# Performance work log

Measured on AMD Instinct MI355X. Metric: run time of the kernel, lower is better.

## Reference

```python
import jax, jax.numpy as jnp
import numpy as np

MARGIN = 0.8  # TripletMarginMiner(margin=0.8, type_of_triplets='semihard')
Z_DIM = 512
N_CONCEPT = 64
NUM_TASK, NUM_SHOT, NUM_WAY = 16, 5, 5


def _triplet_indices(num_shot, num_way):
    # labels = torch.arange(num_way).repeat(num_shot) -> tile pattern
    labels = np.tile(np.arange(num_way), num_shot)
    N = labels.shape[0]
    same = labels[:, None] == labels[None, :]
    pos = same & ~np.eye(N, dtype=bool)          # a != p, same label
    neg = ~same                                  # different label
    a, p, n = np.nonzero(pos[:, :, None] & neg[:, None, :])  # all candidate triplets
    return jnp.asarray(a), jnp.asarray(p), jnp.asarray(n)


def setup_inputs() -> dict:
    key = jax.random.key(0)
    ks = jax.random.split(key, 12)
    d = Z_DIM
    s = lambda fan: 1.0 / np.sqrt(fan)
    inp = {
        'input_data': jax.random.normal(ks[0], (NUM_TASK, NUM_SHOT, NUM_WAY, d), jnp.float32),
        # proj_inner: Linear(3d -> 2d), ReLU, Linear(2d -> d)
        'W1': jax.random.normal(ks[1], (3 * d, 2 * d), jnp.float32) * s(3 * d),
        'b1': jnp.zeros((2 * d,), jnp.float32),
        'W2': jax.random.normal(ks[2], (2 * d, d), jnp.float32) * s(2 * d),
        'b2': jnp.zeros((d,), jnp.float32),
        # proj_outer: Linear(d -> 2d), ReLU, Linear(2d -> d)
        'W3': jax.random.normal(ks[3], (d, 2 * d), jnp.float32) * s(d),
        'b3': jnp.zeros((2 * d,), jnp.float32),
        'W4': jax.random.normal(ks[4], (2 * d, d), jnp.float32) * s(2 * d),
        'b4': jnp.zeros((d,), jnp.float32),
        # cls: Linear(d -> n_concept)
        'Wc': jax.random.normal(ks[5], (d, N_CONCEPT), jnp.float32) * s(d),
        'bc': jnp.zeros((N_CONCEPT,), jnp.float32),
    }
    return inp


def reference(input_data, W1, b1, W2, b2, W3, b3, W4, b4, Wc, bc):
    num_task, num_shot, num_way, d = input_data.shape
    x = input_data.reshape(num_task, num_shot * num_way, d)  # [K, N, d]
    a, p, n = _triplet_indices(num_shot, num_way)            # fixed triplet set [T]

    # --- semihard mining (no grad; binary mask so no grad path anyway) ---
    # LpDistance default: normalize embeddings, then L2 distance
    xn = x / jnp.linalg.norm(x, axis=-1, keepdims=True)
    sq = jnp.sum(xn * xn, axis=-1)                           # [K, N]
    D2 = sq[:, :, None] + sq[:, None, :] - 2.0 * jnp.einsum('kid,kjd->kij', xn, xn)
    D = jnp.sqrt(jnp.clip(D2, 0.0))                          # [K, N, N]
    tm = D[:, a, n] - D[:, a, p]                             # an_dist - ap_dist, [K, T]
    mask = ((tm > 0.0) & (tm <= MARGIN)).astype(x.dtype)     # semihard: 0 < margin <= 0.8

    # --- gather triplet embeddings (unnormalized), concat [x_a, x_p, x_n] ---
    feat = jnp.concatenate([x[:, a], x[:, p], x[:, n]], axis=-1)  # [K, T, 3d]

    # proj_inner then masked sum over mined triplets per task
    h = jax.nn.relu(feat @ W1 + b1) @ W2 + b2                # [K, T, d]
    pooled = jnp.einsum('ktd,kt->kd', h, mask)               # [K, d]

    o = jax.nn.relu(pooled @ W3 + b3) @ W4 + b4              # [K, d]
    score = o @ Wc + bc                                      # [K, n_concept]
    return jax.nn.softmax(score, axis=-1)
```

## Files before the change

### kernel.cpp

```cpp
#include <hip/hip_runtime.h>
#include <math.h>

#define NT 16
#define NR 25
#define DZ 512
#define D2Z 1024
#define NC 64

typedef short bf16x8 __attribute__((ext_vector_type(8)));
typedef float f32x4  __attribute__((ext_vector_type(4)));

#define TP  76
#define XSP 520
#define CP  68

static __device__ inline unsigned short f2bf(float v) {
    union { float f; unsigned u; } x; x.f = v;
    unsigned r = x.u + 0x7fffu + ((x.u >> 16) & 1u);
    return (unsigned short)(r >> 16);
}
static __device__ inline float bf2f(unsigned short h) {
    union { float f; unsigned u; } x; x.u = ((unsigned)h) << 16; return x.f;
}

__global__ __launch_bounds__(256) void k_prep(
    const float* __restrict__ x, const float* __restrict__ W1,
    unsigned short* __restrict__ W1h, unsigned short* __restrict__ W1l,
    float* __restrict__ Dm)
{
    __shared__ unsigned short th[64 * TP], tl[64 * TP];
    int vb = blockIdx.x;
    int tid = threadIdx.x;

    if (vb < 384) {
        int jt = vb & 15;
        int rs = vb >> 4;
        int r0 = rs * 64;
        int j0 = jt * 64;
        int c  = r0 >> 9;
        int rb = r0 & 511;

        #pragma unroll
        for (int it = 0; it < 4; it++) {
            int rl = (tid >> 4) + it * 16;
            int jj = (tid & 15) * 4;
            float4 v = *(const float4*)(W1 + (size_t)(r0 + rl) * D2Z + j0 + jj);
            unsigned short h0 = f2bf(v.x), h1 = f2bf(v.y), h2 = f2bf(v.z), h3 = f2bf(v.w);
            th[rl * TP + jj + 0] = h0; tl[rl * TP + jj + 0] = f2bf(v.x - bf2f(h0));
            th[rl * TP + jj + 1] = h1; tl[rl * TP + jj + 1] = f2bf(v.y - bf2f(h1));
            th[rl * TP + jj + 2] = h2; tl[rl * TP + jj + 2] = f2bf(v.z - bf2f(h2));
            th[rl * TP + jj + 3] = h3; tl[rl * TP + jj + 3] = f2bf(v.w - bf2f(h3));
        }
        __syncthreads();

        #pragma unroll
        for (int it = 0; it < 4; it++) {
            int jl = (tid >> 4) + it * 16;
            int r4 = (tid & 15) * 4;
            ushort4 hv = make_ushort4(th[(r4+0)*TP + jl], th[(r4+1)*TP + jl],
                                      th[(r4+2)*TP + jl], th[(r4+3)*TP + jl]);
            ushort4 lv = make_ushort4(tl[(r4+0)*TP + jl], tl[(r4+1)*TP + jl],
                                      tl[(r4+2)*TP + jl], tl[(r4+3)*TP + jl]);
            size_t dst = ((size_t)c * D2Z + j0 + jl) * DZ + rb + r4;
            *(ushort4*)(W1h + dst) = hv;
            *(ushort4*)(W1l + dst) = lv;
        }
    } else {
        int i = vb - 384;
        int k = i & 15, a = i >> 4;
        int lane = tid & 63;
        int w    = tid >> 6;
        const float* xk = x + (size_t)k * NR * DZ;

        const float4* xap = (const float4*)(xk + a * DZ);
        float4 a0 = xap[lane];
        float4 a1 = xap[lane + 64];

        float sa = a0.x*a0.x + a0.y*a0.y + a0.z*a0.z + a0.w*a0.w
                 + a1.x*a1.x + a1.y*a1.y + a1.z*a1.z + a1.w*a1.w;
        #pragma unroll
        for (int off = 32; off; off >>= 1) sa += __shfl_xor(sa, off);
        float inva = 1.0f / sqrtf(sa);
        a0.x *= inva; a0.y *= inva; a0.z *= inva; a0.w *= inva;
        a1.x *= inva; a1.y *= inva; a1.z *= inva; a1.w *= inva;
        float sqa = a0.x*a0.x + a0.y*a0.y + a0.z*a0.z + a0.w*a0.w
                  + a1.x*a1.x + a1.y*a1.y + a1.z*a1.z + a1.w*a1.w;
        #pragma unroll
        for (int off = 32; off; off >>= 1) sqa += __shfl_xor(sqa, off);

        for (int j = w; j < NR; j += 4) {
            const float4* xjp = (const float4*)(xk + j * DZ);
            float4 j0 = xjp[lane];
            float4 j1 = xjp[lane + 64];
            float sj = j0.x*j0.x + j0.y*j0.y + j0.z*j0.z + j0.w*j0.w
                     + j1.x*j1.x + j1.y*j1.y + j1.z*j1.z + j1.w*j1.w;
            #pragma unroll
            for (int off = 32; off; off >>= 1) sj += __shfl_xor(sj, off);
            float invj = 1.0f / sqrtf(sj);
            j0.x *= invj; j0.y *= invj; j0.z *= invj; j0.w *= invj;
            j1.x *= invj; j1.y *= invj; j1.z *= invj; j1.w *= invj;

            float sqj = j0.x*j0.x + j0.y*j0.y + j0.z*j0.z + j0.w*j0.w
                      + j1.x*j1.x + j1.y*j1.y + j1.z*j1.z + j1.w*j1.w;
            float dij = a0.x*j0.x + a0.y*j0.y + a0.z*j0.z + a0.w*j0.w
                      + a1.x*j1.x + a1.y*j1.y + a1.z*j1.z + a1.w*j1.w;
            #pragma unroll
            for (int off = 32; off; off >>= 1) {
                sqj += __shfl_xor(sqj, off);
                dij += __shfl_xor(dij, off);
            }
            float d2 = sqa + sqj - 2.0f * dij;
            float d  = sqrtf(fmaxf(d2, 0.0f));
            if (lane == 0) Dm[((size_t)k * NR + a) * NR + j] = d;
        }
    }
}

__global__ __launch_bounds__(1024) void k_fused(
    const float* __restrict__ x,
    const unsigned short* __restrict__ W1h, const unsigned short* __restrict__ W1l,
    const float* __restrict__ b1, const float* __restrict__ Dm,
    float* __restrict__ G, float* __restrict__ cnt)
{
    __shared__ unsigned short xs_h[25 * XSP], xs_l[25 * XSP];
    __shared__ float Ct[4][75 * CP];
    __shared__ float Dm_s[NR * NR];
    __shared__ float red[16][64];
    __shared__ float cred[4];

    int bid = blockIdx.x;
    int k  = bid >> 4;
    int jt = bid & 15;
    int j0 = jt * 64;

    int tid  = threadIdx.x;
    int lane = tid & 63;
    int w    = tid >> 6;
    int g    = w & 3;
    int kh   = w >> 2;
    int q    = lane >> 4;
    int ln16 = lane & 15;

    for (int idx = tid; idx < NR * NR; idx += 1024)
        Dm_s[idx] = Dm[(size_t)k * NR * NR + idx];

    for (int gi = tid; gi < NR * 64; gi += 1024) {
        int row = gi >> 6;
        int c8  = (gi & 63) * 8;
        const float* xp = x + ((size_t)k * NR + row) * DZ + c8;
        float4 v0 = *(const float4*)(xp);
        float4 v1 = *(const float4*)(xp + 4);
        unsigned short h;
        ushort4 ha, hb, la, lb;
        h = f2bf(v0.x); ha.x = h; la.x = f2bf(v0.x - bf2f(h));
        h = f2bf(v0.y); ha.y = h; la.y = f2bf(v0.y - bf2f(h));
        h = f2bf(v0.z); ha.z = h; la.z = f2bf(v0.z - bf2f(h));
        h = f2bf(v0.w); ha.w = h; la.w = f2bf(v0.w - bf2f(h));
        h = f2bf(v1.x); hb.x = h; lb.x = f2bf(v1.x - bf2f(h));
        h = f2bf(v1.y); hb.y = h; lb.y = f2bf(v1.y - bf2f(h));
        h = f2bf(v1.z); hb.z = h; lb.z = f2bf(v1.z - bf2f(h));
        h = f2bf(v1.w); hb.w = h; lb.w = f2bf(v1.w - bf2f(h));
        *(ushort4*)&xs_h[row * XSP + c8]     = ha;
        *(ushort4*)&xs_h[row * XSP + c8 + 4] = hb;
        *(ushort4*)&xs_l[row * XSP + c8]     = la;
        *(ushort4*)&xs_l[row * XSP + c8 + 4] = lb;
    }
    __syncthreads();

    if (jt == 0 && tid < 256) {
        float cntv = 0.0f;
        for (int idx = tid; idx < 2000; idx += 256) {
            int a   = idx / 80;
            int rem = idx - a * 80;
            int mi  = rem / 20;
            int nn  = rem - mi * 20;
            int qa = a % 5, mdiv = a / 5;
            int m = mi + (mi >= mdiv);
            int p = qa + 5 * m;
            int ng = nn >> 2, o = nn & 3;
            int n = ng * 5 + o + (o >= qa);
            float tm = Dm_s[a * NR + n] - Dm_s[a * NR + p];
            cntv += ((tm > 0.0f) && (tm <= 0.8f)) ? 1.0f : 0.0f;
        }
        #pragma unroll
        for (int off = 32; off; off >>= 1) cntv += __shfl_xor(cntv, off);
        if (lane == 0) cred[w] = cntv;
    }

    int rowA1 = 16 + ln16;
    if (rowA1 > 24) rowA1 = 24;

    const unsigned short* wb_h = W1h + ((size_t)j0 + g * 16 + ln16) * DZ + q * 8;
    const unsigned short* wb_l = W1l + ((size_t)j0 + g * 16 + ln16) * DZ + q * 8;

    for (int c = 0; c < 3; c++) {
        f32x4 acc0 = (f32x4){0.f,0.f,0.f,0.f};
        f32x4 acc1 = (f32x4){0.f,0.f,0.f,0.f};
        const unsigned short* wch = wb_h + (size_t)c * D2Z * DZ;
        const unsigned short* wcl = wb_l + (size_t)c * D2Z * DZ;

        #pragma unroll
        for (int kc2 = 0; kc2 < 4; kc2++) {
            int kc  = kh * 4 + kc2;
            int kog = kc * 32 + q * 8;
            bf16x8 b_h = *(const bf16x8*)(wch + kc * 32);
            bf16x8 b_l = *(const bf16x8*)(wcl + kc * 32);
            bf16x8 a0h = *(const bf16x8*)&xs_h[ln16 * XSP + kog];
            bf16x8 a0l = *(const bf16x8*)&xs_l[ln16 * XSP + kog];
            bf16x8 a1h = *(const bf16x8*)&xs_h[rowA1 * XSP + kog];
            bf16x8 a1l = *(const bf16x8*)&xs_l[rowA1 * XSP + kog];
            acc0 = __builtin_amdgcn_mfma_f32_16x16x32_bf16(a0h, b_h, acc0, 0, 0, 0);
            acc0 = __builtin_amdgcn_mfma_f32_16x16x32_bf16(a0h, b_l, acc0, 0, 0, 0);
            acc0 = __builtin_amdgcn_mfma_f32_16x16x32_bf16(a0l, b_h, acc0, 0, 0, 0);
            acc1 = __builtin_amdgcn_mfma_f32_16x16x32_bf16(a1h, b_h, acc1, 0, 0, 0);
            acc1 = __builtin_amdgcn_mfma_f32_16x16x32_bf16(a1h, b_l, acc1, 0, 0, 0);
            acc1 = __builtin_amdgcn_mfma_f32_16x16x32_bf16(a1l, b_h, acc1, 0, 0, 0);
        }

        int col = g * 16 + ln16;
        #pragma unroll
        for (int r = 0; r < 4; r++) {
            int r0 = q * 4 + r;
            Ct[kh][(c * 25 + r0) * CP + col] = acc0[r];
            int r1 = 16 + q * 4 + r;
            if (r1 < 25) Ct[kh][(c * 25 + r1) * CP + col] = acc1[r];
        }
    }
    __syncthreads();

    if (jt == 0 && tid == 0)
        cnt[k] = cred[0] + cred[1] + cred[2] + cred[3];

    int j  = tid & 63;
    int h  = (tid >> 6) & 3;
    int ag = tid >> 8;
    float b1v = b1[j0 + j];

    float a3v[NR];
    #pragma unroll
    for (int i = 0; i < NR; i++)
        a3v[i] = Ct[0][(50 + i) * CP + j] + Ct[1][(50 + i) * CP + j]
               + Ct[2][(50 + i) * CP + j] + Ct[3][(50 + i) * CP + j];

    float acc = 0.0f;
    #define ACC_BODY(a) { \
        const int qa = (a) % 5, mdiv = (a) / 5; \
        int m = h + (h >= mdiv); \
        int p = qa + 5 * m; \
        float a1v = Ct[0][(a) * CP + j] + Ct[1][(a) * CP + j] \
                  + Ct[2][(a) * CP + j] + Ct[3][(a) * CP + j]; \
        float a2v = Ct[0][(25 + p) * CP + j] + Ct[1][(25 + p) * CP + j] \
                  + Ct[2][(25 + p) * CP + j] + Ct[3][(25 + p) * CP + j]; \
        float dap = Dm_s[(a) * NR + p]; \
        float s = a1v + a2v + b1v; \
        _Pragma("unroll") \
        for (int ng = 0; ng < 5; ng++) { \
            _Pragma("unroll") \
            for (int o = 0; o < 4; o++) { \
                int n = ng * 5 + o + (o >= qa); \
                float tm = Dm_s[(a) * NR + n] - dap; \
                bool sel = (tm > 0.0f) && (tm <= 0.8f); \
                float pre = fmaxf(s + a3v[n], 0.0f); \
                acc = fmaf(sel ? 1.0f : 0.0f, pre, acc); \
            } \
        } }
    if (ag == 0) {
        #pragma unroll
        for (int a = 0; a < 7; a++) ACC_BODY(a)
    } else if (ag == 1) {
        #pragma unroll
        for (int a = 7; a < 13; a++) ACC_BODY(a)
    } else if (ag == 2) {
        #pragma unroll
        for (int a = 13; a < 19; a++) ACC_BODY(a)
    } else {
        #pragma unroll
        for (int a = 19; a < 25; a++) ACC_BODY(a)
    }
    #undef ACC_BODY

    red[tid >> 6][j] = acc;
    __syncthreads();
    if (tid < 64) {
        float s = 0.0f;
        #pragma unroll
        for (int r = 0; r < 16; r++) s += red[r][tid];
        G[(size_t)k * D2Z + j0 + tid] = s;
    }
}


__global__ __launch_bounds__(256) void kA(const float* __restrict__ G,
                                          const float* __restrict__ W2,
                                          float* __restrict__ pp)
{
    __shared__ float GsT[64 * 16];
    __shared__ float red2[4][16][64];
    int jq = blockIdx.x & 15, ct = blockIdx.x >> 4;
    int tid = threadIdx.x;

    for (int idx = tid; idx < 1024; idx += 256) {
        int t = idx & 15, jj = idx >> 4;
        GsT[jj * 16 + t] = G[(size_t)t * D2Z + jq * 64 + jj];
    }
    __syncthreads();

    int cg = tid & 63, sub = tid >> 6;
    int col = ct * 64 + cg;
    float acc[16];
    #pragma unroll
    for (int t = 0; t < 16; t++) acc[t] = 0.0f;

    for (int jj = 0; jj < 16; jj++) {
        int jr = sub * 16 + jj;
        float wv = W2[(size_t)(jq * 64 + jr) * DZ + col];
        const float4* gp = (const float4*)&GsT[jr * 16];
        float4 g0 = gp[0], g1 = gp[1], g2 = gp[2], g3 = gp[3];
        acc[0]  = fmaf(g0.x, wv, acc[0]);  acc[1]  = fmaf(g0.y, wv, acc[1]);
        acc[2]  = fmaf(g0.z, wv, acc[2]);  acc[3]  = fmaf(g0.w, wv, acc[3]);
        acc[4]  = fmaf(g1.x, wv, acc[4]);  acc[5]  = fmaf(g1.y, wv, acc[5]);
        acc[6]  = fmaf(g1.z, wv, acc[6]);  acc[7]  = fmaf(g1.w, wv, acc[7]);
        acc[8]  = fmaf(g2.x, wv, acc[8]);  acc[9]  = fmaf(g2.y, wv, acc[9]);
        acc[10] = fmaf(g2.z, wv, acc[10]); acc[11] = fmaf(g2.w, wv, acc[11]);
        acc[12] = fmaf(g3.x, wv, acc[12]); acc[13] = fmaf(g3.y, wv, acc[13]);
        acc[14] = fmaf(g3.z, wv, acc[14]); acc[15] = fmaf(g3.w, wv, acc[15]);
    }
    #pragma unroll
    for (int t = 0; t < 16; t++) red2[sub][t][cg] = acc[t];
    __syncthreads();
    for (int r = 0; r < 4; r++) {
        int oi = tid + r * 256;
        int t = oi >> 6, c2 = oi & 63;
        float s = red2[0][t][c2] + red2[1][t][c2] + red2[2][t][c2] + red2[3][t][c2];
        pp[(size_t)jq * 8192 + t * DZ + ct * 64 + c2] = s;
    }
}

__global__ __launch_bounds__(256) void kB(const float* __restrict__ pp,
                                          const float* __restrict__ cnt,
                                          const float* __restrict__ b2,
                                          const float* __restrict__ W3,
                                          float* __restrict__ up)
{
    __shared__ float PsT[64 * 16];
    __shared__ float red2[4][16][64];
    int ct = blockIdx.x & 15, cq = blockIdx.x >> 4;
    int tid = threadIdx.x;

    for (int idx = tid; idx < 1024; idx += 256) {
        int t = idx & 15, cl = idx >> 4;
        int c = cq * 64 + cl;
        float v = cnt[t] * b2[c];
        #pragma unroll
        for (int sl = 0; sl < 16; sl++)
            v += pp[(size_t)sl * 8192 + t * DZ + c];
        PsT[cl * 16 + t] = v;
    }
    __syncthreads();

    int cg = tid & 63, sub = tid >> 6;
    int col = ct * 64 + cg;
    float acc[16];
    #pragma unroll
    for (int t = 0; t < 16; t++) acc[t] = 0.0f;

    for (int cl = 0; cl < 16; cl++) {
        int cr = sub * 16 + cl;
        float wv = W3[(size_t)(cq * 64 + cr) * D2Z + col];
        const float4* gp = (const float4*)&PsT[cr * 16];
        float4 g0 = gp[0], g1 = gp[1], g2 = gp[2], g3 = gp[3];
        acc[0]  = fmaf(g0.x, wv, acc[0]);  acc[1]  = fmaf(g0.y, wv, acc[1]);
        acc[2]  = fmaf(g0.z, wv, acc[2]);  acc[3]  = fmaf(g0.w, wv, acc[3]);
        acc[4]  = fmaf(g1.x, wv, acc[4]);  acc[5]  = fmaf(g1.y, wv, acc[5]);
        acc[6]  = fmaf(g1.z, wv, acc[6]);  acc[7]  = fmaf(g1.w, wv, acc[7]);
        acc[8]  = fmaf(g2.x, wv, acc[8]);  acc[9]  = fmaf(g2.y, wv, acc[9]);
        acc[10] = fmaf(g2.z, wv, acc[10]); acc[11] = fmaf(g2.w, wv, acc[11]);
        acc[12] = fmaf(g3.x, wv, acc[12]); acc[13] = fmaf(g3.y, wv, acc[13]);
        acc[14] = fmaf(g3.z, wv, acc[14]); acc[15] = fmaf(g3.w, wv, acc[15]);
    }
    #pragma unroll
    for (int t = 0; t < 16; t++) red2[sub][t][cg] = acc[t];
    __syncthreads();
    for (int r = 0; r < 4; r++) {
        int oi = tid + r * 256;
        int t = oi >> 6, c2 = oi & 63;
        float s = red2[0][t][c2] + red2[1][t][c2] + red2[2][t][c2] + red2[3][t][c2];
        up[(size_t)cq * 16384 + t * D2Z + ct * 64 + c2] = s;
    }
}

__global__ __launch_bounds__(256) void kC(const float* __restrict__ up,
                                          const float* __restrict__ b3,
                                          const float* __restrict__ W4,
                                          float* __restrict__ op)
{
    __shared__ float UsT[64 * 16];
    __shared__ float red2[4][16][64];
    int ct = blockIdx.x & 7, sq = blockIdx.x >> 3;
    int tid = threadIdx.x;

    for (int idx = tid; idx < 1024; idx += 256) {
        int t = idx & 15, sl = idx >> 4;
        int s = sq * 64 + sl;
        float v = b3[s];
        #pragma unroll
        for (int c8 = 0; c8 < 8; c8++)
            v += up[(size_t)c8 * 16384 + t * D2Z + s];
        UsT[sl * 16 + t] = fmaxf(v, 0.0f);
    }
    __syncthreads();

    int cg = tid & 63, sub = tid >> 6;
    int col = ct * 64 + cg;
    float acc[16];
    #pragma unroll
    for (int t = 0; t < 16; t++) acc[t] = 0.0f;

    for (int sl = 0; sl < 16; sl++) {
        int sr = sub * 16 + sl;
        float wv = W4[(size_t)(sq * 64 + sr) * DZ + col];
        const float4* gp = (const float4*)&UsT[sr * 16];
        float4 g0 = gp[0], g1 = gp[1], g2 = gp[2], g3 = gp[3];
        acc[0]  = fmaf(g0.x, wv, acc[0]);  acc[1]  = fmaf(g0.y, wv, acc[1]);
        acc[2]  = fmaf(g0.z, wv, acc[2]);  acc[3]  = fmaf(g0.w, wv, acc[3]);
        acc[4]  = fmaf(g1.x, wv, acc[4]);  acc[5]  = fmaf(g1.y, wv, acc[5]);
        acc[6]  = fmaf(g1.z, wv, acc[6]);  acc[7]  = fmaf(g1.w, wv, acc[7]);
        acc[8]  = fmaf(g2.x, wv, acc[8]);  acc[9]  = fmaf(g2.y, wv, acc[9]);
        acc[10] = fmaf(g2.z, wv, acc[10]); acc[11] = fmaf(g2.w, wv, acc[11]);
        acc[12] = fmaf(g3.x, wv, acc[12]); acc[13] = fmaf(g3.y, wv, acc[13]);
        acc[14] = fmaf(g3.z, wv, acc[14]); acc[15] = fmaf(g3.w, wv, acc[15]);
    }
    #pragma unroll
    for (int t = 0; t < 16; t++) red2[sub][t][cg] = acc[t];
    __syncthreads();
    for (int r = 0; r < 4; r++) {
        int oi = tid + r * 256;
        int t = oi >> 6, c2 = oi & 63;
        float s = red2[0][t][c2] + red2[1][t][c2] + red2[2][t][c2] + red2[3][t][c2];
        op[(size_t)sq * 8192 + t * DZ + ct * 64 + c2] = s;
    }
}

__global__ __launch_bounds__(256) void kD(const float* __restrict__ op,
                                          const float* __restrict__ b4,
                                          const float* __restrict__ Wc,
                                          const float* __restrict__ bc,
                                          float* __restrict__ out)
{
    __shared__ float Os[DZ];
    __shared__ float tmp[4][64];
    int k = blockIdx.x;
    int tid = threadIdx.x;

    for (int c = tid; c < DZ; c += 256) {
        float v = b4[c];
        #pragma unroll
        for (int sl = 0; sl < 16; sl++)
            v += op[(size_t)sl * 8192 + k * DZ + c];
        Os[c] = v;
    }
    __syncthreads();

    int oc = tid & 63, seg = tid >> 6;
    float a0 = 0.f, a1 = 0.f, a2 = 0.f, a3 = 0.f;
    int r0 = seg * 128;
    #pragma unroll 4
    for (int rr = r0; rr < r0 + 128; rr += 4) {
        a0 = fmaf(Os[rr+0], Wc[(size_t)(rr+0) * NC + oc], a0);
        a1 = fmaf(Os[rr+1], Wc[(size_t)(rr+1) * NC + oc], a1);
        a2 = fmaf(Os[rr+2], Wc[(size_t)(rr+2) * NC + oc], a2);
        a3 = fmaf(Os[rr+3], Wc[(size_t)(rr+3) * NC + oc], a3);
    }
    tmp[seg][oc] = (a0 + a1) + (a2 + a3);
    __syncthreads();
    if (tid < 64) {
        float sc = bc[tid] + tmp[0][tid] + tmp[1][tid] + tmp[2][tid] + tmp[3][tid];
        float m = sc;
        #pragma unroll
        for (int off = 32; off; off >>= 1) m = fmaxf(m, __shfl_xor(m, off));
        float e = expf(sc - m);
        float ss = e;
        #pragma unroll
        for (int off = 32; off; off >>= 1) ss += __shfl_xor(ss, off);
        out[k * NC + tid] = e / ss;
    }
}

extern "C" void kernel_launch(void* const* d_in, const int* in_sizes, int n_in,
                              void* d_out, int out_size, void* d_ws, size_t ws_size,
                              hipStream_t stream)
{
    const float* x  = (const float*)d_in[0];
    const float* W1 = (const float*)d_in[1];
    const float* b1 = (const float*)d_in[2];
    const float* W2 = (const float*)d_in[3];
    const float* b2 = (const float*)d_in[4];
    const float* W3 = (const float*)d_in[5];
    const float* b3 = (const float*)d_in[6];
    const float* W4 = (const float*)d_in[7];
    const float* b4 = (const float*)d_in[8];
    const float* Wc = (const float*)d_in[9];
    const float* bc = (const float*)d_in[10];
    float* out = (float*)d_out;

    float* ws   = (float*)d_ws;
    float* Dm   = ws;
    float* cnt  = ws + 10016;
    float* G    = ws + 10032;
    float* pp   = ws + 26416;
    float* up   = ws + 157488;
    float* op   = ws + 288560;
    unsigned short* W1h = (unsigned short*)(ws + 419632);
    unsigned short* W1l = W1h + 3 * D2Z * DZ;

    k_prep <<<784,  256, 0, stream>>>(x, W1, W1h, W1l, Dm);
    k_fused<<<256, 1024, 0, stream>>>(x, W1h, W1l, b1, Dm, G, cnt);
    kA     <<<128,  256, 0, stream>>>(G, W2, pp);
    kB     <<<128,  256, 0, stream>>>(pp, cnt, b2, W3, up);
    kC     <<<128,  256, 0, stream>>>(up, b3, W4, op);
    kD     <<<NT,   256, 0, stream>>>(op, b4, Wc, bc, out);
}
```

Before: 140.1 us.

## Split W1 into bf16 hi/lo inside the fused GEMM instead of a prep pass

Removes the separate W1 transpose and bf16 hi/lo split pass, along with its 12 MB of workspace writes and re-reads. The fused kernel now reads W1 fp32 directly, using column-strided scalar loads, and converts each element to hi/lo bf16 in registers before the MFMAs. The distance computation moves into its own small kernel. In exchange, the fused kernel issues uncoalesced strided global loads (8 rows apart per vector) and does extra conversion ALU work, and every task block repeats that conversion.

```diff
diff --git a/kernel.cpp b/kernel.cpp
--- a/kernel.cpp
+++ b/kernel.cpp
@@ -10,7 +10,6 @@
 typedef short bf16x8 __attribute__((ext_vector_type(8)));
 typedef float f32x4  __attribute__((ext_vector_type(4)));
 
-#define TP  76
 #define XSP 520
 #define CP  68
 
@@ -23,102 +22,61 @@
     union { float f; unsigned u; } x; x.u = ((unsigned)h) << 16; return x.f;
 }
 
-__global__ __launch_bounds__(256) void k_prep(
+__global__ __launch_bounds__(256) void k_dist(
+    const float* __restrict__ x, float* __restrict__ Dm)
+{
+    int i = blockIdx.x;
+    int tid = threadIdx.x;
+    int k = i & 15, a = i >> 4;
+    int lane = tid & 63;
+    int w    = tid >> 6;
+    const float* xk = x + (size_t)k * NR * DZ;
+
+    const float4* xap = (const float4*)(xk + a * DZ);
+    float4 a0 = xap[lane];
+    float4 a1 = xap[lane + 64];
+
+    float sa = a0.x*a0.x + a0.y*a0.y + a0.z*a0.z + a0.w*a0.w
+             + a1.x*a1.x + a1.y*a1.y + a1.z*a1.z + a1.w*a1.w;
+    #pragma unroll
+    for (int off = 32; off; off >>= 1) sa += __shfl_xor(sa, off);
+    float inva = 1.0f / sqrtf(sa);
+    a0.x *= inva; a0.y *= inva; a0.z *= inva; a0.w *= inva;
+    a1.x *= inva; a1.y *= inva; a1.z *= inva; a1.w *= inva;
+    float sqa = a0.x*a0.x + a0.y*a0.y + a0.z*a0.z + a0.w*a0.w
+              + a1.x*a1.x + a1.y*a1.y + a1.z*a1.z + a1.w*a1.w;
+    #pragma unroll
+    for (int off = 32; off; off >>= 1) sqa += __shfl_xor(sqa, off);
+
+    for (int j = w; j < NR; j += 4) {
+        const float4* xjp = (const float4*)(xk + j * DZ);
+        float4 j0 = xjp[lane];
+        float4 j1 = xjp[lane + 64];
+        float sj = j0.x*j0.x + j0.y*j0.y + j0.z*j0.z + j0.w*j0.w
+                 + j1.x*j1.x + j1.y*j1.y + j1.z*j1.z + j1.w*j1.w;
+        #pragma unroll
+        for (int off = 32; off; off >>= 1) sj += __shfl_xor(sj, off);
+        float invj = 1.0f / sqrtf(sj);
+        j0.x *= invj; j0.y *= invj; j0.z *= invj; j0.w *= invj;
+        j1.x *= invj; j1.y *= invj; j1.z *= invj; j1.w *= invj;
+
+        float sqj = j0.x*j0.x + j0.y*j0.y + j0.z*j0.z + j0.w*j0.w
+                  + j1.x*j1.x + j1.y*j1.y + j1.z*j1.z + j1.w*j1.w;
+        float dij = a0.x*j0.x + a0.y*j0.y + a0.z*j0.z + a0.w*j0.w
+                  + a1.x*j1.x + a1.y*j1.y + a1.z*j1.z + a1.w*j1.w;
+        #pragma unroll
+        for (int off = 32; off; off >>= 1) {
+            sqj += __shfl_xor(sqj, off);
+            dij += __shfl_xor(dij, off);
+        }
+        float d2 = sqa + sqj - 2.0f * dij;
+        float d  = sqrtf(fmaxf(d2, 0.0f));
+        if (lane == 0) Dm[((size_t)k * NR + a) * NR + j] = d;
+    }
+}
+
+__global__ __launch_bounds__(1024) void k_fused(
     const float* __restrict__ x, const float* __restrict__ W1,
-    unsigned short* __restrict__ W1h, unsigned short* __restrict__ W1l,
-    float* __restrict__ Dm)
-{
-    __shared__ unsigned short th[64 * TP], tl[64 * TP];
-    int vb = blockIdx.x;
-    int tid = threadIdx.x;
-
-    if (vb < 384) {
-        int jt = vb & 15;
-        int rs = vb >> 4;
-        int r0 = rs * 64;
-        int j0 = jt * 64;
-        int c  = r0 >> 9;
-        int rb = r0 & 511;
-
-        #pragma unroll
-        for (int it = 0; it < 4; it++) {
-            int rl = (tid >> 4) + it * 16;
-            int jj = (tid & 15) * 4;
-            float4 v = *(const float4*)(W1 + (size_t)(r0 + rl) * D2Z + j0 + jj);
-            unsigned short h0 = f2bf(v.x), h1 = f2bf(v.y), h2 = f2bf(v.z), h3 = f2bf(v.w);
-            th[rl * TP + jj + 0] = h0; tl[rl * TP + jj + 0] = f2bf(v.x - bf2f(h0));
-            th[rl * TP + jj + 1] = h1; tl[rl * TP + jj + 1] = f2bf(v.y - bf2f(h1));
-            th[rl * TP + jj + 2] = h2; tl[rl * TP + jj + 2] = f2bf(v.z - bf2f(h2));
-            th[rl * TP + jj + 3] = h3; tl[rl * TP + jj + 3] = f2bf(v.w - bf2f(h3));
-        }
-        __syncthreads();
-
-        #pragma unroll
-        for (int it = 0; it < 4; it++) {
-            int jl = (tid >> 4) + it * 16;
-            int r4 = (tid & 15) * 4;
-            ushort4 hv = make_ushort4(th[(r4+0)*TP + jl], th[(r4+1)*TP + jl],
-                                      th[(r4+2)*TP + jl], th[(r4+3)*TP + jl]);
-            ushort4 lv = make_ushort4(tl[(r4+0)*TP + jl], tl[(r4+1)*TP + jl],
-                                      tl[(r4+2)*TP + jl], tl[(r4+3)*TP + jl]);
-            size_t dst = ((size_t)c * D2Z + j0 + jl) * DZ + rb + r4;
-            *(ushort4*)(W1h + dst) = hv;
-            *(ushort4*)(W1l + dst) = lv;
-        }
-    } else {
-        int i = vb - 384;
-        int k = i & 15, a = i >> 4;
-        int lane = tid & 63;
-        int w    = tid >> 6;
-        const float* xk = x + (size_t)k * NR * DZ;
-
-        const float4* xap = (const float4*)(xk + a * DZ);
-        float4 a0 = xap[lane];
-        float4 a1 = xap[lane + 64];
-
-        float sa = a0.x*a0.x + a0.y*a0.y + a0.z*a0.z + a0.w*a0.w
-                 + a1.x*a1.x + a1.y*a1.y + a1.z*a1.z + a1.w*a1.w;
-        #pragma unroll
-        for (int off = 32; off; off >>= 1) sa += __shfl_xor(sa, off);
-        float inva = 1.0f / sqrtf(sa);
-        a0.x *= inva; a0.y *= inva; a0.z *= inva; a0.w *= inva;
-        a1.x *= inva; a1.y *= inva; a1.z *= inva; a1.w *= inva;
-        float sqa = a0.x*a0.x + a0.y*a0.y + a0.z*a0.z + a0.w*a0.w
-                  + a1.x*a1.x + a1.y*a1.y + a1.z*a1.z + a1.w*a1.w;
-        #pragma unroll
-        for (int off = 32; off; off >>= 1) sqa += __shfl_xor(sqa, off);
-
-        for (int j = w; j < NR; j += 4) {
-            const float4* xjp = (const float4*)(xk + j * DZ);
-            float4 j0 = xjp[lane];
-            float4 j1 = xjp[lane + 64];
-            float sj = j0.x*j0.x + j0.y*j0.y + j0.z*j0.z + j0.w*j0.w
-                     + j1.x*j1.x + j1.y*j1.y + j1.z*j1.z + j1.w*j1.w;
-            #pragma unroll
-            for (int off = 32; off; off >>= 1) sj += __shfl_xor(sj, off);
-            float invj = 1.0f / sqrtf(sj);
-            j0.x *= invj; j0.y *= invj; j0.z *= invj; j0.w *= invj;
-            j1.x *= invj; j1.y *= invj; j1.z *= invj; j1.w *= invj;
-
-            float sqj = j0.x*j0.x + j0.y*j0.y + j0.z*j0.z + j0.w*j0.w
-                      + j1.x*j1.x + j1.y*j1.y + j1.z*j1.z + j1.w*j1.w;
-            float dij = a0.x*j0.x + a0.y*j0.y + a0.z*j0.z + a0.w*j0.w
-                      + a1.x*j1.x + a1.y*j1.y + a1.z*j1.z + a1.w*j1.w;
-            #pragma unroll
-            for (int off = 32; off; off >>= 1) {
-                sqj += __shfl_xor(sqj, off);
-                dij += __shfl_xor(dij, off);
-            }
-            float d2 = sqa + sqj - 2.0f * dij;
-            float d  = sqrtf(fmaxf(d2, 0.0f));
-            if (lane == 0) Dm[((size_t)k * NR + a) * NR + j] = d;
-        }
-    }
-}
-
-__global__ __launch_bounds__(1024) void k_fused(
-    const float* __restrict__ x,
-    const unsigned short* __restrict__ W1h, const unsigned short* __restrict__ W1l,
     const float* __restrict__ b1, const float* __restrict__ Dm,
     float* __restrict__ G, float* __restrict__ cnt)
 {
@@ -190,21 +148,26 @@
     int rowA1 = 16 + ln16;
     if (rowA1 > 24) rowA1 = 24;
 
-    const unsigned short* wb_h = W1h + ((size_t)j0 + g * 16 + ln16) * DZ + q * 8;
-    const unsigned short* wb_l = W1l + ((size_t)j0 + g * 16 + ln16) * DZ + q * 8;
+    const float* wcol = W1 + (size_t)(kh * 128 + q * 8) * D2Z + (j0 + g * 16 + ln16);
 
     for (int c = 0; c < 3; c++) {
         f32x4 acc0 = (f32x4){0.f,0.f,0.f,0.f};
         f32x4 acc1 = (f32x4){0.f,0.f,0.f,0.f};
-        const unsigned short* wch = wb_h + (size_t)c * D2Z * DZ;
-        const unsigned short* wcl = wb_l + (size_t)c * D2Z * DZ;
+        const float* wc = wcol + (size_t)c * DZ * D2Z;
 
         #pragma unroll
         for (int kc2 = 0; kc2 < 4; kc2++) {
             int kc  = kh * 4 + kc2;
             int kog = kc * 32 + q * 8;
-            bf16x8 b_h = *(const bf16x8*)(wch + kc * 32);
-            bf16x8 b_l = *(const bf16x8*)(wcl + kc * 32);
+            const float* bp = wc + (size_t)kc2 * 32 * D2Z;
+            bf16x8 b_h, b_l;
+            #pragma unroll
+            for (int i2 = 0; i2 < 8; i2++) {
+                float v = bp[(size_t)i2 * D2Z];
+                unsigned short hh = f2bf(v);
+                b_h[i2] = (short)hh;
+                b_l[i2] = (short)f2bf(v - bf2f(hh));
+            }
             bf16x8 a0h = *(const bf16x8*)&xs_h[ln16 * XSP + kog];
             bf16x8 a0l = *(const bf16x8*)&xs_l[ln16 * XSP + kog];
             bf16x8 a1h = *(const bf16x8*)&xs_h[rowA1 * XSP + kog];
@@ -510,11 +473,9 @@
     float* pp   = ws + 26416;
     float* up   = ws + 157488;
     float* op   = ws + 288560;
-    unsigned short* W1h = (unsigned short*)(ws + 419632);
-    unsigned short* W1l = W1h + 3 * D2Z * DZ;
-
-    k_prep <<<784,  256, 0, stream>>>(x, W1, W1h, W1l, Dm);
-    k_fused<<<256, 1024, 0, stream>>>(x, W1h, W1l, b1, Dm, G, cnt);
+
+    k_dist <<<400,  256, 0, stream>>>(x, Dm);
+    k_fused<<<256, 1024, 0, stream>>>(x, W1, b1, Dm, G, cnt);
     kA     <<<128,  256, 0, stream>>>(G, W2, pp);
     kB     <<<128,  256, 0, stream>>>(pp, cnt, b2, W3, up);
     kC     <<<128,  256, 0, stream>>>(up, b3, W4, op);
```

Result: faster. 133.2 us (-4.9%).
